# Kernel tuning notes

Hardware: AMD Instinct MI355X
Metric: run time of the kernel (lower is better)

The kernel has to match this reference:

```python
import jax, jax.numpy as jnp
import numpy as np
from jax import lax

N, E, IN, OUT, H, OH = 2048, 16384, 128, 128, 4, 8
NEG_SLOPE = 0.2

def symlog(v):
    return jnp.sign(v) * jnp.log1p(jnp.abs(v))

def setup_inputs() -> dict:
    key = jax.random.key(0)
    ks = jax.random.split(key, 16)
    x = jax.random.normal(ks[0], (N, IN), dtype=jnp.float32)
    onehot = jax.random.uniform(ks[1], (N, N), dtype=jnp.float32)
    src = jax.random.randint(ks[2], (E,), 0, N, dtype=jnp.int32)
    # guarantee no self loops (original removes them before adding its own)
    off = jax.random.randint(ks[3], (E,), 1, N, dtype=jnp.int32)
    dst = (src + off) % N
    s = 0.05
    lin_w = jax.random.normal(ks[4], (H * OUT, IN + OH), dtype=jnp.float32) * s
    att_l = jax.random.normal(ks[5], (1, H, OUT), dtype=jnp.float32) * s
    att_r = jax.random.normal(ks[6], (1, H, OUT), dtype=jnp.float32) * s
    bias = jnp.zeros((H * OUT,), dtype=jnp.float32)
    conv1_w = jax.random.normal(ks[7], (8, 1, 3), dtype=jnp.float32) * s
    conv1_b = jnp.zeros((8,), dtype=jnp.float32)
    conv2_w = jax.random.normal(ks[8], (16, 8, 3), dtype=jnp.float32) * s
    conv2_b = jnp.zeros((16,), dtype=jnp.float32)
    fc_w = jax.random.normal(ks[9], (OH, 16), dtype=jnp.float32) * s
    fc_b = jnp.zeros((OH,), dtype=jnp.float32)
    return {"x": x, "onehot": onehot, "src": src, "dst": dst,
            "lin_w": lin_w, "att_l": att_l, "att_r": att_r, "bias": bias,
            "conv1_w": conv1_w, "conv1_b": conv1_b, "conv2_w": conv2_w,
            "conv2_b": conv2_b, "fc_w": fc_w, "fc_b": fc_b}

def _forward(x, onehot, src, dst, lin_w, att_l, att_r, bias,
             conv1_w, conv1_b, conv2_w, conv2_b, fc_w, fc_b):
    n = x.shape[0]
    # --- one-hot conv pipeline: sort -> symlog -> Conv1d x2 -> avgpool -> Linear ---
    prep = symlog(jnp.sort(onehot, axis=-1))[:, None, :]          # [N,1,N]
    dn = ('NCH', 'OIH', 'NCH')
    h = lax.conv_general_dilated(prep, conv1_w, (1,), [(1, 1)], dimension_numbers=dn)
    h = jax.nn.relu(h + conv1_b[None, :, None])                    # [N,8,N]
    h = lax.conv_general_dilated(h, conv2_w, (1,), [(1, 1)], dimension_numbers=dn)
    h = jax.nn.relu(h + conv2_b[None, :, None])                    # [N,16,N]
    pooled = h.mean(axis=-1)                                       # AdaptiveAvgPool1d(1) -> [N,16]
    oh_feat = pooled @ fc_w.T + fc_b                               # [N,OH]
    # --- linear + per-head attention logits ---
    xh = (jnp.concatenate([x, oh_feat], axis=-1) @ lin_w.T).reshape(n, H, OUT)
    sa = (xh * att_l).sum(-1)                                      # [N,H]
    ra = (xh * att_r).sum(-1)
    # --- add self loops (input edges contain none) ---
    loop = jnp.arange(n, dtype=src.dtype)
    s_i = jnp.concatenate([src, loop])
    d_i = jnp.concatenate([dst, loop])
    # --- message: LeakyReLU attention * one-hot dot attention ---
    alpha = jax.nn.leaky_relu(sa[s_i] + ra[d_i], NEG_SLOPE)        # [E',H]
    send_oh = onehot[s_i]                                          # [E',N]
    dotatt = 1.0 / ((symlog(send_oh) * symlog(onehot[d_i])).sum(axis=1) + 1.0)
    alpha = alpha * dotatt[:, None]
    # --- segment softmax over receiving node ---
    amax = jax.ops.segment_max(alpha, d_i, num_segments=n)
    ex = jnp.exp(alpha - amax[d_i])
    den = jax.ops.segment_sum(ex, d_i, num_segments=n)
    alpha = ex / (den[d_i] + 1e-16)
    # --- weighted aggregate (scatter-sum) ---
    agg_x = jax.ops.segment_sum(xh[s_i] * alpha[:, :, None], d_i, num_segments=n)
    agg_oh = jax.ops.segment_sum(send_oh, d_i, num_segments=n)
    new_x = agg_x.reshape(n, H * OUT) + bias                       # concat heads + bias
    new_onehot = onehot + agg_oh                                   # one_hot_incay='add'
    return new_x, new_onehot

def reference(x, onehot, src, dst, lin_w, att_l, att_r, bias,
              conv1_w, conv1_b, conv2_w, conv2_b, fc_w, fc_b):
    return _forward(x, onehot, src, dst, lin_w, att_l, att_r, bias,
                    conv1_w, conv1_b, conv2_w, conv2_b, fc_w, fc_b)
```

## Files before the change

kernel.cpp:

```cpp
#include <hip/hip_runtime.h>
#include <math.h>

#define NN   2048
#define NE   16384
#define NET  (NE + NN)
#define INF_ 128
#define OUTF 128
#define NH   4
#define OHF  8
#define NEG_SLOPE 0.2f
#define CAP  512

__device__ __forceinline__ float symlogf_(float v) {
    return copysignf(__logf(1.0f + fabsf(v)), v);
}

__global__ __launch_bounds__(256, 2) void k_sortconv(
    const float* __restrict__ onehot,
    const float* __restrict__ c1w, const float* __restrict__ c1b,
    const float* __restrict__ c2w, const float* __restrict__ c2b,
    const float* __restrict__ fcw, const float* __restrict__ fcb,
    float* __restrict__ slog, float* __restrict__ ohfeat) {
    __shared__ float soa[NN];
    __shared__ float bndL[4][2];
    __shared__ float bndR[4][2];
    __shared__ float red[64];
    __shared__ float pooled[16];
    const int t = threadIdx.x;
    const int r = blockIdx.x;
    const int b = t << 3;
    const int wave = t >> 6, lane = t & 63;
    const float* row  = onehot + (size_t)r * NN;
    float*       srow = slog   + (size_t)r * NN;

    float4 lo = ((const float4*)row)[t * 2];
    float4 hi = ((const float4*)row)[t * 2 + 1];
    float v[8] = {lo.x, lo.y, lo.z, lo.w, hi.x, hi.y, hi.z, hi.w};
    {
        float4 s0, s1;
        s0.x = symlogf_(v[0]); s0.y = symlogf_(v[1]);
        s0.z = symlogf_(v[2]); s0.w = symlogf_(v[3]);
        s1.x = symlogf_(v[4]); s1.y = symlogf_(v[5]);
        s1.z = symlogf_(v[6]); s1.w = symlogf_(v[7]);
        ((float4*)srow)[t * 2]     = s0;
        ((float4*)srow)[t * 2 + 1] = s1;
    }

    auto cx = [](float& x, float& y, bool up) {
        float mn = fminf(x, y), mx = fmaxf(x, y);
        x = up ? mn : mx;
        y = up ? mx : mn;
    };

    cx(v[0], v[1], true);  cx(v[2], v[3], false);
    cx(v[4], v[5], true);  cx(v[6], v[7], false);
    cx(v[0], v[2], true);  cx(v[1], v[3], true);
    cx(v[4], v[6], false); cx(v[5], v[7], false);
    cx(v[0], v[1], true);  cx(v[2], v[3], true);
    cx(v[4], v[5], false); cx(v[6], v[7], false);
    {
        const bool u8 = ((t & 1) == 0);
        cx(v[0], v[4], u8); cx(v[1], v[5], u8); cx(v[2], v[6], u8); cx(v[3], v[7], u8);
        cx(v[0], v[2], u8); cx(v[1], v[3], u8); cx(v[4], v[6], u8); cx(v[5], v[7], u8);
        cx(v[0], v[1], u8); cx(v[2], v[3], u8); cx(v[4], v[5], u8); cx(v[6], v[7], u8);
    }

    for (int k = 16; k <= NN; k <<= 1) {
        const bool up = ((b & k) == 0);
        for (int j = k >> 1; j >= 8; j >>= 1) {
            const int pj = j >> 3;
            const bool keepmin = (((t & pj) == 0) == up);
            if (pj <= 32) {
                #pragma unroll
                for (int e = 0; e < 8; e++) {
                    float p = __shfl_xor(v[e], pj, 64);
                    v[e] = keepmin ? fminf(v[e], p) : fmaxf(v[e], p);
                }
            } else {
                __syncthreads();
                #pragma unroll
                for (int e = 0; e < 8; e++) soa[e * 256 + t] = v[e];
                __syncthreads();
                const int pt = t ^ pj;
                #pragma unroll
                for (int e = 0; e < 8; e++) {
                    float p = soa[e * 256 + pt];
                    v[e] = keepmin ? fminf(v[e], p) : fmaxf(v[e], p);
                }
            }
        }
        cx(v[0], v[4], up); cx(v[1], v[5], up); cx(v[2], v[6], up); cx(v[3], v[7], up);
        cx(v[0], v[2], up); cx(v[1], v[3], up); cx(v[4], v[6], up); cx(v[5], v[7], up);
        cx(v[0], v[1], up); cx(v[2], v[3], up); cx(v[4], v[5], up); cx(v[6], v[7], up);
    }

    #pragma unroll
    for (int e = 0; e < 8; e++) v[e] = symlogf_(v[e]);

    __syncthreads();
    if (lane == 63) { bndL[wave][0] = v[6]; bndL[wave][1] = v[7]; }
    if (lane == 0)  { bndR[wave][0] = v[0]; bndR[wave][1] = v[1]; }
    __syncthreads();
    float vm2 = __shfl_up(v[6], 1, 64);
    float vm1 = __shfl_up(v[7], 1, 64);
    float vp8 = __shfl_down(v[0], 1, 64);
    float vp9 = __shfl_down(v[1], 1, 64);
    if (lane == 0) {
        vm2 = wave ? bndL[wave - 1][0] : 0.0f;
        vm1 = wave ? bndL[wave - 1][1] : 0.0f;
    }
    if (lane == 63) {
        vp8 = (wave < 3) ? bndR[wave + 1][0] : 0.0f;
        vp9 = (wave < 3) ? bndR[wave + 1][1] : 0.0f;
    }

    float vin[12];
    vin[0] = vm2; vin[1] = vm1;
    #pragma unroll
    for (int e = 0; e < 8; e++) vin[2 + e] = v[e];
    vin[10] = vp8; vin[11] = vp9;

    float h1c[10][8];
    {
        float w1[24], b1[8];
        #pragma unroll
        for (int q = 0; q < 24; q++) w1[q] = c1w[q];
        #pragma unroll
        for (int q = 0; q < 8; q++)  b1[q] = c1b[q];
        #pragma unroll
        for (int m = 0; m < 10; m++) {
            const float xm = vin[m], xc = vin[m + 1], xp = vin[m + 2];
            #pragma unroll
            for (int c = 0; c < 8; c++) {
                float a = fmaf(w1[c * 3 + 2], xp,
                          fmaf(w1[c * 3 + 1], xc,
                          fmaf(w1[c * 3 + 0], xm, b1[c])));
                h1c[m][c] = fmaxf(a, 0.0f);
            }
        }
        if (t == 0) {
            #pragma unroll
            for (int c = 0; c < 8; c++) h1c[0][c] = 0.0f;
        }
        if (t == 255) {
            #pragma unroll
            for (int c = 0; c < 8; c++) h1c[9][c] = 0.0f;
        }
    }

    float sums[16];
    #pragma unroll
    for (int ch = 0; ch < 16; ch++) {
        float wch[24];
        #pragma unroll
        for (int q = 0; q < 24; q++) wch[q] = c2w[ch * 24 + q];
        const float bb = c2b[ch];
        float acc = 0.0f;
        #pragma unroll
        for (int i = 0; i < 8; i++) {
            float a = bb;
            #pragma unroll
            for (int c = 0; c < 8; c++) {
                a = fmaf(wch[c * 3 + 0], h1c[i][c],     a);
                a = fmaf(wch[c * 3 + 1], h1c[i + 1][c], a);
                a = fmaf(wch[c * 3 + 2], h1c[i + 2][c], a);
            }
            acc += fmaxf(a, 0.0f);
        }
        sums[ch] = acc;
    }

    #pragma unroll
    for (int c = 0; c < 16; c++)
        for (int o = 32; o; o >>= 1) sums[c] += __shfl_down(sums[c], o);
    if (lane == 0)
        #pragma unroll
        for (int c = 0; c < 16; c++) red[wave * 16 + c] = sums[c];
    __syncthreads();
    if (t < 16)
        pooled[t] = (red[t] + red[16 + t] + red[32 + t] + red[48 + t]) * (1.0f / NN);
    __syncthreads();
    if (t < OHF) {
        float a = fcb[t];
        #pragma unroll
        for (int c = 0; c < 16; c++) a = fmaf(fcw[t * 16 + c], pooled[c], a);
        ohfeat[r * OHF + t] = a;
    }
}

__global__ __launch_bounds__(256) void k_xh(
    const float* __restrict__ x, const float* __restrict__ ohf,
    const float* __restrict__ lin_w, const float* __restrict__ att_l,
    const float* __restrict__ att_r, float* __restrict__ xh,
    float* __restrict__ sa, float* __restrict__ ra) {
    const int n0 = blockIdx.x * 4;
    __shared__ float xin[4][136];
    __shared__ float part[4][16];
    const int tid = threadIdx.x;
    const int wave = tid >> 6, lane = tid & 63;
    for (int i = tid; i < 4 * 136; i += 256) {
        int nn = i / 136, k = i - nn * 136;
        xin[nn][k] = (k < INF_) ? x[(size_t)(n0+nn)*INF_ + k]
                                : ohf[(n0+nn)*OHF + (k - INF_)];
    }
    __syncthreads();
    float accl[2][4], accr[2][4];
    #pragma unroll
    for (int g = 0; g < 2; g++)
        #pragma unroll
        for (int n = 0; n < 4; n++) { accl[g][n] = 0.0f; accr[g][n] = 0.0f; }

    #pragma unroll
    for (int g = 0; g < 2; g++) {
        const int o = tid + g * 256;
        const float4* wr4 = (const float4*)(lin_w + (size_t)o * 136);
        float a0 = 0, a1 = 0, a2 = 0, a3 = 0;
        for (int kk = 0; kk < 34; kk++) {
            float4 w = wr4[kk];
            int k = kk * 4;
            a0 += w.x*xin[0][k] + w.y*xin[0][k+1] + w.z*xin[0][k+2] + w.w*xin[0][k+3];
            a1 += w.x*xin[1][k] + w.y*xin[1][k+1] + w.z*xin[1][k+2] + w.w*xin[1][k+3];
            a2 += w.x*xin[2][k] + w.y*xin[2][k+1] + w.z*xin[2][k+2] + w.w*xin[2][k+3];
            a3 += w.x*xin[3][k] + w.y*xin[3][k+1] + w.z*xin[3][k+2] + w.w*xin[3][k+3];
        }
        xh[(size_t)(n0+0)*512 + o] = a0;
        xh[(size_t)(n0+1)*512 + o] = a1;
        xh[(size_t)(n0+2)*512 + o] = a2;
        xh[(size_t)(n0+3)*512 + o] = a3;
        const float al = att_l[o], ar = att_r[o];
        accl[g][0] = fmaf(a0, al, accl[g][0]); accr[g][0] = fmaf(a0, ar, accr[g][0]);
        accl[g][1] = fmaf(a1, al, accl[g][1]); accr[g][1] = fmaf(a1, ar, accr[g][1]);
        accl[g][2] = fmaf(a2, al, accl[g][2]); accr[g][2] = fmaf(a2, ar, accr[g][2]);
        accl[g][3] = fmaf(a3, al, accl[g][3]); accr[g][3] = fmaf(a3, ar, accr[g][3]);
    }
    #pragma unroll
    for (int g = 0; g < 2; g++)
        #pragma unroll
        for (int n = 0; n < 4; n++)
            for (int o = 32; o; o >>= 1) {
                accl[g][n] += __shfl_down(accl[g][n], o);
                accr[g][n] += __shfl_down(accr[g][n], o);
            }
    if (lane == 0) {
        #pragma unroll
        for (int g = 0; g < 2; g++)
            #pragma unroll
            for (int n = 0; n < 4; n++) {
                part[wave][n * 4 + g * 2 + 0] = accl[g][n];
                part[wave][n * 4 + g * 2 + 1] = accr[g][n];
            }
    }
    __syncthreads();
    if (tid < 32) {
        const int n = tid >> 3, rem = tid & 7, h = rem >> 1, lr = rem & 1;
        const int g = h >> 1, wp = (h & 1) * 2;
        const float val = part[wp][n * 4 + g * 2 + lr] + part[wp + 1][n * 4 + g * 2 + lr];
        if (lr == 0) sa[(n0 + n) * 4 + h] = val;
        else         ra[(n0 + n) * 4 + h] = val;
    }
}

__global__ void k_count(const int* __restrict__ dst, int* __restrict__ deg) {
    int e = blockIdx.x * 256 + threadIdx.x;
    if (e < NET) {
        int d = (e < NE) ? dst[e] : (e - NE);
        atomicAdd(&deg[d], 1);
    }
}

__global__ __launch_bounds__(256) void k_scan(
    const int* __restrict__ deg, int* __restrict__ csr_off,
    int* __restrict__ csr_pos) {
    __shared__ int wsum[4];
    const int t = threadIdx.x, wave = t >> 6, lane = t & 63;
    int loc[8], s = 0;
    #pragma unroll
    for (int k = 0; k < 8; k++) { loc[k] = deg[t*8 + k]; s += loc[k]; }
    int x = s;
    for (int o = 1; o < 64; o <<= 1) {
        int u = __shfl_up(x, o, 64);
        if (lane >= o) x += u;
    }
    if (lane == 63) wsum[wave] = x;
    __syncthreads();
    int off = 0;
    #pragma unroll
    for (int w = 0; w < 4; w++) if (w < wave) off += wsum[w];
    int base = off + x - s;
    #pragma unroll
    for (int k = 0; k < 8; k++) {
        csr_off[t*8 + k] = base;
        csr_pos[t*8 + k] = base;
        base += loc[k];
    }
    if (t == 255) csr_off[NN] = off + x;
}

__global__ void k_fill(const int* __restrict__ dst, int* __restrict__ csr_pos,
                       int* __restrict__ csr_e) {
    int e = blockIdx.x * 256 + threadIdx.x;
    if (e < NET) {
        int d = (e < NE) ? dst[e] : (e - NE);
        int pos = atomicAdd(&csr_pos[d], 1);
        csr_e[pos] = e;
    }
}

__global__ __launch_bounds__(256) void k_alpha(
    const int* __restrict__ src, const int* __restrict__ dst,
    const float* __restrict__ slog, const float* __restrict__ sa,
    const float* __restrict__ ra, float* __restrict__ alpha) {
    const int e = blockIdx.x;
    int s, d;
    if (e < NE) { s = src[e]; d = dst[e]; } else { s = d = e - NE; }
    const int tid = threadIdx.x;
    const float4* A = (const float4*)(slog + (size_t)s * NN);
    const float4* B = (const float4*)(slog + (size_t)d * NN);
    float4 a0 = A[tid*2], a1 = A[tid*2 + 1];
    float4 b0 = B[tid*2], b1 = B[tid*2 + 1];
    float p = a0.x*b0.x + a0.y*b0.y + a0.z*b0.z + a0.w*b0.w
            + a1.x*b1.x + a1.y*b1.y + a1.z*b1.z + a1.w*b1.w;
    for (int o = 32; o; o >>= 1) p += __shfl_down(p, o);
    __shared__ float ps[4];
    const int wave = tid >> 6, lane = tid & 63;
    if (lane == 0) ps[wave] = p;
    __syncthreads();
    if (tid == 0) {
        float dot  = ps[0] + ps[1] + ps[2] + ps[3];
        float datt = 1.0f / (dot + 1.0f);
        float4 out;
        float* po = (float*)&out;
        for (int h = 0; h < 4; h++) {
            float a = sa[s*4 + h] + ra[d*4 + h];
            a = (a >= 0.0f) ? a : NEG_SLOPE * a;
            po[h] = a * datt;
        }
        *(float4*)(alpha + (size_t)e * 4) = out;
    }
}

__global__ __launch_bounds__(256) void k_soft_aggx(
    const int* __restrict__ src, const int* __restrict__ csr_off,
    const int* __restrict__ csr_e, const float* __restrict__ alpha,
    const float* __restrict__ xh, const float* __restrict__ bias,
    float* __restrict__ out_x) {
    const int d = blockIdx.x;
    const int begin = csr_off[d];
    int deg = csr_off[d + 1] - begin;
    if (deg > CAP) deg = CAP;
    __shared__ float wls[CAP * 4];
    __shared__ int   sls[CAP];
    const int tid = threadIdx.x;
    for (int t = tid; t < deg; t += 256) {
        int e = csr_e[begin + t];
        sls[t] = (e < NE) ? src[e] : (e - NE);
        float4 a = *(const float4*)(alpha + (size_t)e * 4);
        wls[t*4 + 0] = a.x; wls[t*4 + 1] = a.y;
        wls[t*4 + 2] = a.z; wls[t*4 + 3] = a.w;
    }
    __syncthreads();
    const int wave = tid >> 6, lane = tid & 63;
    if (wave < 4) {
        float m = -3.4e38f;
        for (int t = lane; t < deg; t += 64) m = fmaxf(m, wls[t*4 + wave]);
        for (int o = 32; o; o >>= 1) m = fmaxf(m, __shfl_down(m, o));
        m = __shfl(m, 0);
        float s = 0.0f;
        for (int t = lane; t < deg; t += 64) {
            float ex = expf(wls[t*4 + wave] - m);
            wls[t*4 + wave] = ex;
            s += ex;
        }
        for (int o = 32; o; o >>= 1) s += __shfl_down(s, o);
        s = __shfl(s, 0);
        float inv = 1.0f / (s + 1e-16f);
        for (int t = lane; t < deg; t += 64) wls[t*4 + wave] *= inv;
    }
    __syncthreads();
    for (int ho = tid; ho < 512; ho += 256) {
        const int h = ho >> 7;
        float acc = 0.0f;
        for (int t = 0; t < deg; t++)
            acc += wls[t*4 + h] * xh[(size_t)sls[t] * 512 + ho];
        out_x[(size_t)d * 512 + ho] = acc + bias[ho];
    }
}

__global__ __launch_bounds__(256) void k_aggoh(
    const float* __restrict__ onehot, const int* __restrict__ src,
    const int* __restrict__ csr_off, const int* __restrict__ csr_e,
    float* __restrict__ out_oh) {
    const int d = blockIdx.x;
    const int begin = csr_off[d], end = csr_off[d + 1];
    const int tid = threadIdx.x;
    const float4* own = (const float4*)(onehot + (size_t)d * NN);
    float4 A = own[tid], B = own[tid + 256];
    for (int p = begin; p < end; p++) {
        int e = csr_e[p];
        int s = (e < NE) ? src[e] : (e - NE);
        const float4* r4 = (const float4*)(onehot + (size_t)s * NN);
        float4 u = r4[tid], v = r4[tid + 256];
        A.x += u.x; A.y += u.y; A.z += u.z; A.w += u.w;
        B.x += v.x; B.y += v.y; B.z += v.z; B.w += v.w;
    }
    float4* o4 = (float4*)(out_oh + (size_t)d * NN);
    o4[tid] = A; o4[tid + 256] = B;
}

extern "C" void kernel_launch(void* const* d_in, const int* in_sizes, int n_in,
                              void* d_out, int out_size, void* d_ws, size_t ws_size,
                              hipStream_t stream) {
    const float* x      = (const float*)d_in[0];
    const float* onehot = (const float*)d_in[1];
    const int*   src    = (const int*)d_in[2];
    const int*   dst    = (const int*)d_in[3];
    const float* lin_w  = (const float*)d_in[4];
    const float* att_l  = (const float*)d_in[5];
    const float* att_r  = (const float*)d_in[6];
    const float* bias   = (const float*)d_in[7];
    const float* c1w    = (const float*)d_in[8];
    const float* c1b    = (const float*)d_in[9];
    const float* c2w    = (const float*)d_in[10];
    const float* c2b    = (const float*)d_in[11];
    const float* fcw    = (const float*)d_in[12];
    const float* fcb    = (const float*)d_in[13];

    float* out_x  = (float*)d_out;
    float* out_oh = out_x + (size_t)NN * (NH * OUTF);

    float* ws    = (float*)d_ws;
    float* slog  = ws;
    float* xh    = slog + (size_t)NN * NN;
    float* ohf   = xh   + (size_t)NN * 512;
    float* sa    = ohf  + (size_t)NN * OHF;
    float* ra    = sa   + (size_t)NN * NH;
    float* alpha = ra   + (size_t)NN * NH;
    int* deg     = (int*)(alpha + (size_t)NET * 4);
    int* csr_off = deg + NN;
    int* csr_pos = csr_off + NN + 1;
    int* csr_e   = csr_pos + NN;

    hipMemsetAsync(deg, 0, NN * sizeof(int), stream);
    k_sortconv<<<NN, 256, 0, stream>>>(onehot, c1w, c1b, c2w, c2b, fcw, fcb, slog, ohf);
    k_count<<<(NET + 255) / 256, 256, 0, stream>>>(dst, deg);
    k_scan<<<1, 256, 0, stream>>>(deg, csr_off, csr_pos);
    k_fill<<<(NET + 255) / 256, 256, 0, stream>>>(dst, csr_pos, csr_e);
    k_xh<<<NN / 4, 256, 0, stream>>>(x, ohf, lin_w, att_l, att_r, xh, sa, ra);
    k_alpha<<<NET, 256, 0, stream>>>(src, dst, slog, sa, ra, alpha);
    k_soft_aggx<<<NN, 256, 0, stream>>>(src, csr_off, csr_e, alpha, xh, bias, out_x);
    k_aggoh<<<NN, 256, 0, stream>>>(onehot, src, csr_off, csr_e, out_oh);
}
```

Baseline: 292.2 us.

## Compute dot-attention per wave and fuse softmax, x and onehot aggregation

The per-edge dot-attention kernel now computes one edge per wave instead of one per 256-thread block. The leaky-relu and attention-logit math moves into the aggregation kernel, so k_datt only stores a scalar per edge. The x aggregation and the onehot aggregation are merged into one per-destination kernel that walks the edge list once. That kernel uses float2 loads for xh, which removes a kernel launch, the alpha round trip and a second pass over the CSR list. In exchange the fused kernel holds more registers, and when the degree exceeds CAP the onehot aggregation is now truncated too, where the old onehot kernel summed every neighbour.

```diff
diff --git a/kernel.cpp b/kernel.cpp
--- a/kernel.cpp
+++ b/kernel.cpp
@@ -306,44 +306,35 @@
     }
 }
 
-__global__ __launch_bounds__(256) void k_alpha(
+__global__ __launch_bounds__(256) void k_datt(
     const int* __restrict__ src, const int* __restrict__ dst,
-    const float* __restrict__ slog, const float* __restrict__ sa,
-    const float* __restrict__ ra, float* __restrict__ alpha) {
-    const int e = blockIdx.x;
+    const float* __restrict__ slog, float* __restrict__ datt) {
+    const int e = blockIdx.x * 4 + (threadIdx.x >> 6);
+    const int lane = threadIdx.x & 63;
     int s, d;
     if (e < NE) { s = src[e]; d = dst[e]; } else { s = d = e - NE; }
-    const int tid = threadIdx.x;
     const float4* A = (const float4*)(slog + (size_t)s * NN);
     const float4* B = (const float4*)(slog + (size_t)d * NN);
-    float4 a0 = A[tid*2], a1 = A[tid*2 + 1];
-    float4 b0 = B[tid*2], b1 = B[tid*2 + 1];
-    float p = a0.x*b0.x + a0.y*b0.y + a0.z*b0.z + a0.w*b0.w
-            + a1.x*b1.x + a1.y*b1.y + a1.z*b1.z + a1.w*b1.w;
+    float p = 0.0f;
+    #pragma unroll
+    for (int i = 0; i < 8; i++) {
+        float4 a = A[lane + 64 * i];
+        float4 b = B[lane + 64 * i];
+        p = fmaf(a.x, b.x, p); p = fmaf(a.y, b.y, p);
+        p = fmaf(a.z, b.z, p); p = fmaf(a.w, b.w, p);
+    }
+    #pragma unroll
     for (int o = 32; o; o >>= 1) p += __shfl_down(p, o);
-    __shared__ float ps[4];
-    const int wave = tid >> 6, lane = tid & 63;
-    if (lane == 0) ps[wave] = p;
-    __syncthreads();
-    if (tid == 0) {
-        float dot  = ps[0] + ps[1] + ps[2] + ps[3];
-        float datt = 1.0f / (dot + 1.0f);
-        float4 out;
-        float* po = (float*)&out;
-        for (int h = 0; h < 4; h++) {
-            float a = sa[s*4 + h] + ra[d*4 + h];
-            a = (a >= 0.0f) ? a : NEG_SLOPE * a;
-            po[h] = a * datt;
-        }
-        *(float4*)(alpha + (size_t)e * 4) = out;
-    }
-}
-
-__global__ __launch_bounds__(256) void k_soft_aggx(
+    if (lane == 0) datt[e] = 1.0f / (p + 1.0f);
+}
+
+__global__ __launch_bounds__(256) void k_agg(
     const int* __restrict__ src, const int* __restrict__ csr_off,
-    const int* __restrict__ csr_e, const float* __restrict__ alpha,
-    const float* __restrict__ xh, const float* __restrict__ bias,
-    float* __restrict__ out_x) {
+    const int* __restrict__ csr_e, const float* __restrict__ datt,
+    const float* __restrict__ sa, const float* __restrict__ ra,
+    const float* __restrict__ xh, const float* __restrict__ onehot,
+    const float* __restrict__ bias, float* __restrict__ out_x,
+    float* __restrict__ out_oh) {
     const int d = blockIdx.x;
     const int begin = csr_off[d];
     int deg = csr_off[d + 1] - begin;
@@ -351,16 +342,23 @@
     __shared__ float wls[CAP * 4];
     __shared__ int   sls[CAP];
     const int tid = threadIdx.x;
+    const float4 rav = *(const float4*)(ra + d * 4);
     for (int t = tid; t < deg; t += 256) {
         int e = csr_e[begin + t];
-        sls[t] = (e < NE) ? src[e] : (e - NE);
-        float4 a = *(const float4*)(alpha + (size_t)e * 4);
-        wls[t*4 + 0] = a.x; wls[t*4 + 1] = a.y;
-        wls[t*4 + 2] = a.z; wls[t*4 + 3] = a.w;
+        int s = (e < NE) ? src[e] : (e - NE);
+        sls[t] = s;
+        float4 sav = *(const float4*)(sa + s * 4);
+        float dt = datt[e];
+        float a0 = sav.x + rav.x; a0 = (a0 >= 0.0f ? a0 : NEG_SLOPE * a0) * dt;
+        float a1 = sav.y + rav.y; a1 = (a1 >= 0.0f ? a1 : NEG_SLOPE * a1) * dt;
+        float a2 = sav.z + rav.z; a2 = (a2 >= 0.0f ? a2 : NEG_SLOPE * a2) * dt;
+        float a3 = sav.w + rav.w; a3 = (a3 >= 0.0f ? a3 : NEG_SLOPE * a3) * dt;
+        wls[t*4 + 0] = a0; wls[t*4 + 1] = a1;
+        wls[t*4 + 2] = a2; wls[t*4 + 3] = a3;
     }
     __syncthreads();
     const int wave = tid >> 6, lane = tid & 63;
-    if (wave < 4) {
+    {
         float m = -3.4e38f;
         for (int t = lane; t < deg; t += 64) m = fmaxf(m, wls[t*4 + wave]);
         for (int o = 32; o; o >>= 1) m = fmaxf(m, __shfl_down(m, o));
@@ -377,32 +375,26 @@
         for (int t = lane; t < deg; t += 64) wls[t*4 + wave] *= inv;
     }
     __syncthreads();
-    for (int ho = tid; ho < 512; ho += 256) {
-        const int h = ho >> 7;
-        float acc = 0.0f;
-        for (int t = 0; t < deg; t++)
-            acc += wls[t*4 + h] * xh[(size_t)sls[t] * 512 + ho];
-        out_x[(size_t)d * 512 + ho] = acc + bias[ho];
-    }
-}
-
-__global__ __launch_bounds__(256) void k_aggoh(
-    const float* __restrict__ onehot, const int* __restrict__ src,
-    const int* __restrict__ csr_off, const int* __restrict__ csr_e,
-    float* __restrict__ out_oh) {
-    const int d = blockIdx.x;
-    const int begin = csr_off[d], end = csr_off[d + 1];
-    const int tid = threadIdx.x;
+    const int h = tid >> 6;
+    float2 accx; accx.x = 0.0f; accx.y = 0.0f;
     const float4* own = (const float4*)(onehot + (size_t)d * NN);
     float4 A = own[tid], B = own[tid + 256];
-    for (int p = begin; p < end; p++) {
-        int e = csr_e[p];
-        int s = (e < NE) ? src[e] : (e - NE);
-        const float4* r4 = (const float4*)(onehot + (size_t)s * NN);
-        float4 u = r4[tid], v = r4[tid + 256];
-        A.x += u.x; A.y += u.y; A.z += u.z; A.w += u.w;
-        B.x += v.x; B.y += v.y; B.z += v.z; B.w += v.w;
-    }
+    const float2* xh2 = (const float2*)xh;
+    const float4* oh4 = (const float4*)onehot;
+    for (int t = 0; t < deg; t++) {
+        const float w = wls[t*4 + h];
+        const int s = sls[t];
+        float2 xv = xh2[(size_t)s * 256 + tid];
+        accx.x = fmaf(w, xv.x, accx.x);
+        accx.y = fmaf(w, xv.y, accx.y);
+        float4 u  = oh4[(size_t)s * 512 + tid];
+        float4 vv = oh4[(size_t)s * 512 + 256 + tid];
+        A.x += u.x;  A.y += u.y;  A.z += u.z;  A.w += u.w;
+        B.x += vv.x; B.y += vv.y; B.z += vv.z; B.w += vv.w;
+    }
+    float2 bv = ((const float2*)bias)[tid];
+    float2 outv; outv.x = accx.x + bv.x; outv.y = accx.y + bv.y;
+    ((float2*)out_x)[(size_t)d * 256 + tid] = outv;
     float4* o4 = (float4*)(out_oh + (size_t)d * NN);
     o4[tid] = A; o4[tid + 256] = B;
 }
@@ -434,8 +426,8 @@
     float* ohf   = xh   + (size_t)NN * 512;
     float* sa    = ohf  + (size_t)NN * OHF;
     float* ra    = sa   + (size_t)NN * NH;
-    float* alpha = ra   + (size_t)NN * NH;
-    int* deg     = (int*)(alpha + (size_t)NET * 4);
+    float* datt  = ra   + (size_t)NN * NH;
+    int* deg     = (int*)(datt + (size_t)NET);
     int* csr_off = deg + NN;
     int* csr_pos = csr_off + NN + 1;
     int* csr_e   = csr_pos + NN;
@@ -446,7 +438,7 @@
     k_scan<<<1, 256, 0, stream>>>(deg, csr_off, csr_pos);
     k_fill<<<(NET + 255) / 256, 256, 0, stream>>>(dst, csr_pos, csr_e);
     k_xh<<<NN / 4, 256, 0, stream>>>(x, ohf, lin_w, att_l, att_r, xh, sa, ra);
-    k_alpha<<<NET, 256, 0, stream>>>(src, dst, slog, sa, ra, alpha);
-    k_soft_aggx<<<NN, 256, 0, stream>>>(src, csr_off, csr_e, alpha, xh, bias, out_x);
-    k_aggoh<<<NN, 256, 0, stream>>>(onehot, src, csr_off, csr_e, out_oh);
-}
+    k_datt<<<NET / 4, 256, 0, stream>>>(src, dst, slog, datt);
+    k_agg<<<NN, 256, 0, stream>>>(src, csr_off, csr_e, datt, sa, ra, xh, onehot,
+                                  bias, out_x, out_oh);
+}
```

Result: no change. 292.1 us (-0.0%).
